# Optimization experiments

Hardware: AMD Instinct MI355X
Metric: run time of the kernel (lower is better)

The kernel has to match this reference:

```python
import jax, jax.numpy as jnp
import numpy as np

N_INPUTS = 128
N_LATENT = 21
LEN_TIME = 51
NUM_SHIFTS = 50
BATCH = 2048
N_HIDDEN = 4  # hidden relu layers in the outer DenseResBlock


def setup_inputs() -> dict:
    key = jax.random.key(0)
    ks = jax.random.split(key, 8)
    s = 0.05  # small init scale keeps activations sane through the residual stack
    return {
        "inputs": jax.random.normal(ks[0], (BATCH, LEN_TIME, N_INPUTS), jnp.float32),
        "L": jnp.eye(N_LATENT, dtype=jnp.float32)
             + s * jax.random.normal(ks[1], (N_LATENT, N_LATENT), jnp.float32),
        "ienc_W": s * jax.random.normal(ks[2], (N_INPUTS, N_LATENT), jnp.float32),
        "idec_W": s * jax.random.normal(ks[3], (N_LATENT, N_INPUTS), jnp.float32),
        "enc_W": s * jax.random.normal(ks[4], (N_HIDDEN, N_INPUTS, N_INPUTS), jnp.float32),
        "enc_b": jnp.zeros((N_HIDDEN, N_INPUTS), jnp.float32),
        "enc_Wo": s * jax.random.normal(ks[5], (N_INPUTS, N_INPUTS), jnp.float32),
        "enc_bo": jnp.zeros((N_INPUTS,), jnp.float32),
        "dec_W": s * jax.random.normal(ks[6], (N_HIDDEN, N_INPUTS, N_INPUTS), jnp.float32),
        "dec_b": jnp.zeros((N_HIDDEN, N_INPUTS), jnp.float32),
        "dec_Wo": s * jax.random.normal(ks[7], (N_INPUTS, N_INPUTS), jnp.float32),
        "dec_bo": jnp.zeros((N_INPUTS,), jnp.float32),
    }


def _resblock(x, W, b, Wo, bo):
    # DenseResBlock: stack of relu Dense layers + linear output + residual skip.
    h = x
    for i in range(W.shape[0]):  # fixed small layer count
        h = jax.nn.relu(h @ W[i] + b[i])
    return x + h @ Wo + bo


def reference(inputs, L, ienc_W, idec_W, enc_W, enc_b, enc_Wo, enc_bo,
              dec_W, dec_b, dec_Wo, dec_bo):
    B, T, n_in = inputs.shape
    len_pred = T - NUM_SHIFTS  # = 1

    auto_in = inputs.reshape(-1, n_in)                        # [B*T, n_in]
    pred_in = inputs[:, :len_pred, :].reshape(-1, n_in)       # [B*len_pred, n_in]

    # autoencoder path
    pe = _resblock(auto_in, enc_W, enc_b, enc_Wo, enc_bo)     # partially encoded
    fe = pe @ ienc_W                                          # fully encoded [., n_latent]
    pd = fe @ idec_W                                          # partially decoded
    autoencoder_output = _resblock(pd, dec_W, dec_b, dec_Wo, dec_bo)
    outer_auto_output = _resblock(pe, dec_W, dec_b, dec_Wo, dec_bo)

    # latent rollout: z_{k+1} = z_k @ L, decode every step
    pe_pred = _resblock(pred_in, enc_W, enc_b, enc_Wo, enc_bo)
    z0 = pe_pred @ ienc_W                                     # [B*len_pred, n_latent]

    def step(z, _):
        z_next = z @ L
        return z_next, z_next

    _, zs = jax.lax.scan(step, z0, None, length=NUM_SHIFTS)   # [S, B*len_pred, n_latent]

    # decode all shifts in one large batched pass (same math as per-shift decode)
    dec_in = zs.reshape(-1, zs.shape[-1]) @ idec_W            # [S*B*len_pred, n_in]
    dec_all = _resblock(dec_in, dec_W, dec_b, dec_Wo, dec_bo)
    predictions = (dec_all
                   .reshape(NUM_SHIFTS, B, len_pred, n_in)
                   .transpose(1, 0, 2, 3)
                   .reshape(B, NUM_SHIFTS * len_pred, n_in))

    return autoencoder_output, outer_auto_output, predictions
```

## Files before the change

kernel.cpp:

```cpp
#include <hip/hip_runtime.h>

#define NF 128
#define NLAT 21
#define NBATCH 2048
#define LEN_T 51
#define NSHIFT 50
#define AUTO_ROWS (NBATCH*LEN_T)
#define PRED_ROWS (NBATCH*NSHIFT)

typedef short bh8  __attribute__((ext_vector_type(8)));
typedef unsigned short us8 __attribute__((ext_vector_type(8)));
typedef float f32x4  __attribute__((ext_vector_type(4)));
typedef float f32x16 __attribute__((ext_vector_type(16)));

#define MFMA32(A,B,C) __builtin_amdgcn_mfma_f32_32x32x16_bf16(A,B,C,0,0,0)
#define SGB(m,n) __builtin_amdgcn_sched_group_barrier((m),(n),0)

__device__ __forceinline__ float bf2f(short s){
  unsigned u = ((unsigned)(unsigned short)s) << 16;
  return __builtin_bit_cast(float, u);
}
__device__ __forceinline__ short f2bf(float v){
  unsigned u = __builtin_bit_cast(unsigned, v);
  return (short)((u + 0x7FFFu + ((u>>16)&1u)) >> 16);
}

__global__ void k_mmul(const float* __restrict__ ienc, const float* __restrict__ idec,
                       float* __restrict__ M){
  int idx = blockIdx.x*256 + threadIdx.x;
  int i = idx>>7, j = idx&127;
  float s = 0.f;
#pragma unroll
  for(int k=0;k<NLAT;++k) s = fmaf(ienc[i*NLAT+k], idec[k*NF+j], s);
  M[idx] = s;
}

__global__ void k_prep(const float* __restrict__ encW, const float* __restrict__ encWo,
                       const float* __restrict__ decW, const float* __restrict__ decWo,
                       const float* __restrict__ M,    const float* __restrict__ idec,
                       unsigned short* __restrict__ swz){
  int id  = blockIdx.x*256 + threadIdx.x;
  int mat = id >> 11;
  int rem = id & 2047;
  int f   = rem >> 6, l = rem & 63;
  int s   = f >> 2,  mt = f & 3;
  int hl  = l >> 5,  c  = l & 31;
  const float* src;
  if(mat<4)       src = encW + mat*16384;
  else if(mat==4) src = encWo;
  else if(mat<9)  src = decW + (mat-5)*16384;
  else if(mat==9) src = decWo;
  else if(mat==10)src = M;
  else            src = idec;
  us8 w8;
#pragma unroll
  for(int i=0;i<8;++i){
    int k = s*16 + 4*hl + (i&3) + 8*(i>>2);
    float v;
    if(mat==11) v = (k<NLAT) ? src[k*NF + mt*32 + c] : 0.f;
    else        v = src[k*NF + mt*32 + c];
    w8[i] = (unsigned short)f2bf(v);
  }
  *(us8*)(swz + (size_t)mat*16384 + (size_t)f*512 + (size_t)l*8) = w8;
}

__device__ __forceinline__ void stage_issue(const unsigned short* g,
                                            unsigned short* lds, int wid, int lane){
  const unsigned short* gp = g + wid*512 + lane*8;
  unsigned short* lp = lds + wid*512;
#pragma unroll
  for(int i=0;i<8;++i){
    __builtin_amdgcn_global_load_lds(
      (const __attribute__((address_space(1))) void*)(gp + i*2048),
      (__attribute__((address_space(3))) void*)(lp + i*2048), 16, 0, 0);
  }
}

__device__ __forceinline__ void ldw4(const unsigned short* wl, int s, int lane, bh8 w[4]){
#pragma unroll
  for(int mt=0;mt<4;++mt) w[mt] = *(const bh8*)(wl + (s*4+mt)*512 + lane*8);
}
__device__ __forceinline__ void mm4(const bh8 w[4], bh8 b, f32x16 acc[4]){
#pragma unroll
  for(int mt=0;mt<4;++mt) acc[mt]=MFMA32(w[mt],b,acc[mt]);
}
__device__ __forceinline__ void run_layer(const unsigned short* wl,
    const bh8 h[8], f32x16 acc[4], int lane){
#pragma unroll
  for(int mt=0;mt<4;++mt){
    f32x16 z;
#pragma unroll
    for(int r=0;r<16;++r) z[r]=0.f;
    acc[mt]=z;
  }
  bh8 wA[4], wB[4];
  ldw4(wl,0,lane,wA);   SGB(0x100,4);
  ldw4(wl,1,lane,wB);   SGB(0x100,4);
  mm4(wA,h[0],acc);     SGB(0x8,4);
  ldw4(wl,2,lane,wA);   SGB(0x100,4);
  mm4(wB,h[1],acc);     SGB(0x8,4);
  ldw4(wl,3,lane,wB);   SGB(0x100,4);
  mm4(wA,h[2],acc);     SGB(0x8,4);
  ldw4(wl,4,lane,wA);   SGB(0x100,4);
  mm4(wB,h[3],acc);     SGB(0x8,4);
  ldw4(wl,5,lane,wB);   SGB(0x100,4);
  mm4(wA,h[4],acc);     SGB(0x8,4);
  ldw4(wl,6,lane,wA);   SGB(0x100,4);
  mm4(wB,h[5],acc);     SGB(0x8,4);
  ldw4(wl,7,lane,wB);   SGB(0x100,4);
  mm4(wA,h[6],acc);     SGB(0x8,4);
  mm4(wB,h[7],acc);     SGB(0x8,4);
}

__device__ __forceinline__ void epi_hidden(f32x16 acc[4], const float* bias,
    bh8 h[8], int hl){
#pragma unroll
  for(int mt=0;mt<4;++mt){
    f32x16 a = acc[mt];
#pragma unroll
    for(int q=0;q<4;++q){
      f32x4 b = *(const f32x4*)(bias + mt*32 + q*8 + hl*4);
#pragma unroll
      for(int j=0;j<4;++j) a[q*4+j]+=b[j];
    }
#pragma unroll
    for(int r=0;r<16;++r) a[r]=fmaxf(a[r],0.f);
#pragma unroll
    for(int p=0;p<2;++p){
      bh8 o;
#pragma unroll
      for(int i=0;i<8;++i) o[i]=f2bf(a[p*8 + (i>>2)*4 + (i&3)]);
      h[mt*2+p]=o;
    }
  }
}
__device__ __forceinline__ void epi_plain(f32x16 acc[4], bh8 h[8], int hl){
#pragma unroll
  for(int mt=0;mt<4;++mt){
    f32x16 a = acc[mt];
#pragma unroll
    for(int p=0;p<2;++p){
      bh8 o;
#pragma unroll
      for(int i=0;i<8;++i) o[i]=f2bf(a[p*8 + (i>>2)*4 + (i&3)]);
      h[mt*2+p]=o;
    }
  }
}

__device__ __forceinline__ void final_direct(float* __restrict__ rowptr,
    f32x16 acc[4], const float* bo, const bh8 res[8], int hl){
#pragma unroll
  for(int mt=0;mt<4;++mt){
    f32x16 a = acc[mt];
#pragma unroll
    for(int q=0;q<4;++q){
      f32x4 b = *(const f32x4*)(bo + mt*32 + q*8 + hl*4);
#pragma unroll
      for(int j=0;j<4;++j) a[q*4+j]+=b[j];
    }
    bh8 r0 = res[2*mt], r1 = res[2*mt+1];
#pragma unroll
    for(int r=0;r<16;++r){
      int i=((r>>2)&1)*4+(r&3);
      a[r] += bf2f(r<8 ? r0[i] : r1[i]);
    }
#pragma unroll
    for(int q=0;q<4;++q){
      f32x4 w; w[0]=a[q*4+0]; w[1]=a[q*4+1]; w[2]=a[q*4+2]; w[3]=a[q*4+3];
      *(f32x4*)(rowptr + mt*32 + q*8 + hl*4) = w;
    }
  }
}

__device__ __forceinline__ void dec_block(const unsigned short* __restrict__ swz,
    unsigned short (*wlds)[16384], int& cur, const float* bdec,
    bh8 h[8], f32x16 acc[4], const unsigned short* next_g,
    int wid, int lane, int hl){
#pragma unroll 1
  for(int l=0;l<4;++l){
    unsigned short* wc = cur ? wlds[1] : wlds[0];
    unsigned short* wn = cur ? wlds[0] : wlds[1];
    stage_issue(swz + (size_t)(l<3 ? 6+l : 9)*16384, wn, wid, lane);
    run_layer(wc, h, acc, lane);
    epi_hidden(acc, bdec + l*128, h, hl);
    __syncthreads(); cur^=1;
  }
  unsigned short* wc = cur ? wlds[1] : wlds[0];
  unsigned short* wn = cur ? wlds[0] : wlds[1];
  if(next_g) stage_issue(next_g, wn, wid, lane);
  run_layer(wc, h, acc, lane);
}

__global__ __launch_bounds__(256,2)
void k_main2(const float* __restrict__ gin, const unsigned short* __restrict__ swz,
             const float* __restrict__ encB, const float* __restrict__ encBo,
             const float* __restrict__ decB, const float* __restrict__ decBo,
             float* __restrict__ out1, float* __restrict__ out2, float* __restrict__ pe0){
  __shared__ __align__(16) unsigned short wlds[2][16384];
  __shared__ __align__(16) float blds[1280];
  const int tid=threadIdx.x, lane=tid&63, wid=tid>>6;
  const int hl=lane>>5, c31=lane&31;
  const int grow0=blockIdx.x*128;
  const int myrow=grow0 + wid*32 + c31;
  bh8 h[8], res[8];
  f32x16 acc[4];

  stage_issue(swz, wlds[0], wid, lane);
  for(int i=tid;i<512;i+=256) blds[i]      = encB[i];
  for(int i=tid;i<512;i+=256) blds[512+i]  = decB[i];
  if(tid<256) blds[1024+tid] = (tid<128) ? encBo[tid] : decBo[tid-128];

#pragma unroll
  for(int s=0;s<8;++s){
    f32x4 a=*(const f32x4*)(gin + (size_t)myrow*NF + s*16 + 4*hl);
    f32x4 b=*(const f32x4*)(gin + (size_t)myrow*NF + s*16 + 8 + 4*hl);
    bh8 o;
#pragma unroll
    for(int i=0;i<4;++i){ o[i]=f2bf(a[i]); o[i+4]=f2bf(b[i]); }
    h[s]=o; res[s]=o;
  }
  __syncthreads();
  int cur=0;

#pragma unroll 1
  for(int l=0;l<4;++l){
    unsigned short* wc = cur ? wlds[1] : wlds[0];
    unsigned short* wn = cur ? wlds[0] : wlds[1];
    stage_issue(swz + (size_t)(l+1)*16384, wn, wid, lane);
    run_layer(wc, h, acc, lane);
    epi_hidden(acc, blds + l*128, h, hl);
    __syncthreads(); cur^=1;
  }
  {
    unsigned short* wc = cur ? wlds[1] : wlds[0];
    unsigned short* wn = cur ? wlds[0] : wlds[1];
    stage_issue(swz + (size_t)5*16384, wn, wid, lane);
    run_layer(wc, h, acc, lane);
    int bidx = myrow / LEN_T;
    bool isz = (myrow == bidx*LEN_T);
#pragma unroll
    for(int mt=0;mt<4;++mt){
      f32x16 a = acc[mt];
#pragma unroll
      for(int q=0;q<4;++q){
        f32x4 b = *(const f32x4*)(blds + 1024 + mt*32 + q*8 + hl*4);
#pragma unroll
        for(int j=0;j<4;++j) a[q*4+j]+=b[j];
      }
      bh8 r0=res[2*mt], r1=res[2*mt+1];
#pragma unroll
      for(int r=0;r<16;++r){
        int i=((r>>2)&1)*4+(r&3);
        a[r] += bf2f(r<8 ? r0[i] : r1[i]);
      }
      if(isz){
#pragma unroll
        for(int q=0;q<4;++q){
          f32x4 w; w[0]=a[q*4+0]; w[1]=a[q*4+1]; w[2]=a[q*4+2]; w[3]=a[q*4+3];
          *(f32x4*)(pe0 + (size_t)bidx*NF + mt*32 + q*8 + hl*4) = w;
        }
      }
#pragma unroll
      for(int p=0;p<2;++p){
        bh8 o;
#pragma unroll
        for(int i=0;i<8;++i) o[i]=f2bf(a[p*8 + (i>>2)*4 + (i&3)]);
        h[mt*2+p]=o;
      }
    }
#pragma unroll
    for(int s=0;s<8;++s) res[s]=h[s];
    __syncthreads(); cur^=1;
  }

  dec_block(swz, wlds, cur, blds+512, h, acc, swz + (size_t)10*16384, wid, lane, hl);
  final_direct(out2 + (size_t)myrow*NF, acc, blds+1152, res, hl);
  __syncthreads(); cur^=1;

  {
    unsigned short* wc = cur ? wlds[1] : wlds[0];
    unsigned short* wn = cur ? wlds[0] : wlds[1];
    stage_issue(swz + (size_t)5*16384, wn, wid, lane);
    run_layer(wc, res, acc, lane);
    epi_plain(acc, h, hl);
#pragma unroll
    for(int s=0;s<8;++s) res[s]=h[s];
    __syncthreads(); cur^=1;
  }

  dec_block(swz, wlds, cur, blds+512, h, acc, nullptr, wid, lane, hl);
  final_direct(out1 + (size_t)myrow*NF, acc, blds+1152, res, hl);
}

__global__ void k_roll(const float* __restrict__ pe0, const float* __restrict__ ienc,
                       const float* __restrict__ L, float* __restrict__ zs){
  const int tid=threadIdx.x, lane=tid&63, wid=tid>>6, sub=lane&31, half=lane>>5;
  const int row=blockIdx.x*8 + wid*2 + half;
  const bool act = sub < NLAT;
  float Lc[NLAT];
#pragma unroll
  for(int k=0;k<NLAT;++k) Lc[k] = act ? L[k*NLAT+sub] : 0.f;
  float z=0.f;
  if(act){
    const float* pr = pe0 + (size_t)row*NF;
    float s0=0.f,s1=0.f,s2=0.f,s3=0.f;
#pragma unroll 8
    for(int k=0;k<NF;k+=4){
      s0=fmaf(pr[k+0], ienc[(k+0)*NLAT+sub], s0);
      s1=fmaf(pr[k+1], ienc[(k+1)*NLAT+sub], s1);
      s2=fmaf(pr[k+2], ienc[(k+2)*NLAT+sub], s2);
      s3=fmaf(pr[k+3], ienc[(k+3)*NLAT+sub], s3);
    }
    z=(s0+s1)+(s2+s3);
  }
  const int base = half*32;
#pragma unroll 1
  for(int s=0;s<NSHIFT;++s){
    float zn=0.f;
#pragma unroll
    for(int k=0;k<NLAT;++k) zn=fmaf(__shfl(z, base+k, 64), Lc[k], zn);
    z=zn;
    if(act) zs[((size_t)s*NBATCH + row)*NLAT + sub] = z;
  }
}

__global__ __launch_bounds__(256,2)
void k_pred2(const float* __restrict__ zs, const unsigned short* __restrict__ swz,
             const float* __restrict__ decB, const float* __restrict__ decBo,
             float* __restrict__ out3){
  __shared__ __align__(16) unsigned short wlds[2][16384];
  __shared__ __align__(16) float blds[1280];
  const int tid=threadIdx.x, lane=tid&63, wid=tid>>6;
  const int hl=lane>>5, c31=lane&31;
  const int grow0=blockIdx.x*128;
  const int prow=grow0 + wid*32 + c31;
  bh8 h[8], res[8];
  f32x16 acc[4];

  stage_issue(swz + (size_t)11*16384, wlds[0], wid, lane);
  for(int i=tid;i<512;i+=256) blds[512+i] = decB[i];
  if(tid<128) blds[1152+tid] = decBo[tid];

  bh8 zf[2];
  {
    const float* zr = zs + (size_t)prow*NLAT;
#pragma unroll
    for(int s=0;s<2;++s){
      bh8 o;
#pragma unroll
      for(int i=0;i<8;++i){
        int cc = s*16 + 4*hl + (i&3) + 8*(i>>2);
        o[i] = (cc<NLAT) ? f2bf(zr[cc]) : (short)0;
      }
      zf[s]=o;
    }
  }
  __syncthreads();
  int cur=0;

  {
    stage_issue(swz + (size_t)5*16384, wlds[1], wid, lane);
#pragma unroll
    for(int mt=0;mt<4;++mt){
      f32x16 z;
#pragma unroll
      for(int r=0;r<16;++r) z[r]=0.f;
      acc[mt]=z;
    }
    bh8 wA[4], wB[4];
    ldw4(wlds[0],0,lane,wA);  SGB(0x100,4);
    ldw4(wlds[0],1,lane,wB);  SGB(0x100,4);
    mm4(wA,zf[0],acc);        SGB(0x8,4);
    mm4(wB,zf[1],acc);        SGB(0x8,4);
    epi_plain(acc, h, hl);
#pragma unroll
    for(int s=0;s<8;++s) res[s]=h[s];
    __syncthreads(); cur^=1;
  }

  dec_block(swz, wlds, cur, blds+512, h, acc, nullptr, wid, lane, hl);

  int sh = prow >> 11, b = prow & 2047;
  final_direct(out3 + ((size_t)b*NSHIFT + sh)*NF, acc, blds+1152, res, hl);
}

extern "C" void kernel_launch(void* const* d_in, const int* in_sizes, int n_in,
                              void* d_out, int out_size, void* d_ws, size_t ws_size,
                              hipStream_t stream) {
  const float* gin   = (const float*)d_in[0];
  const float* L     = (const float*)d_in[1];
  const float* iencW = (const float*)d_in[2];
  const float* idecW = (const float*)d_in[3];
  const float* encW  = (const float*)d_in[4];
  const float* encB  = (const float*)d_in[5];
  const float* encWo = (const float*)d_in[6];
  const float* encBo = (const float*)d_in[7];
  const float* decW  = (const float*)d_in[8];
  const float* decB  = (const float*)d_in[9];
  const float* decWo = (const float*)d_in[10];
  const float* decBo = (const float*)d_in[11];

  float* out1 = (float*)d_out;
  float* out2 = out1 + (size_t)AUTO_ROWS*NF;
  float* out3 = out2 + (size_t)AUTO_ROWS*NF;

  float* M   = (float*)d_ws;
  float* pe0 = M + 16384;
  float* zs  = pe0 + (size_t)NBATCH*NF;
  unsigned short* swz = (unsigned short*)(zs + (size_t)NSHIFT*NBATCH*NLAT);

  hipLaunchKernelGGL(k_mmul, dim3(64),  dim3(256), 0, stream, iencW, idecW, M);
  hipLaunchKernelGGL(k_prep, dim3(96),  dim3(256), 0, stream, encW, encWo, decW, decWo, M, idecW, swz);
  hipLaunchKernelGGL(k_main2, dim3(AUTO_ROWS/128), dim3(256), 0, stream,
                     gin, swz, encB, encBo, decB, decBo, out1, out2, pe0);
  hipLaunchKernelGGL(k_roll, dim3(NBATCH/8), dim3(256), 0, stream, pe0, iencW, L, zs);
  hipLaunchKernelGGL(k_pred2, dim3(PRED_ROWS/128), dim3(256), 0, stream,
                     zs, swz, decB, decBo, out3);
}
```

Measured before the change: 165.6 us.

## Process 64 rows per wave, stash residuals in output buffers, pack bf16 conversions

```diff
diff --git a/kernel.cpp b/kernel.cpp
--- a/kernel.cpp
+++ b/kernel.cpp
@@ -9,9 +9,11 @@
 #define PRED_ROWS (NBATCH*NSHIFT)
 
 typedef short bh8  __attribute__((ext_vector_type(8)));
+typedef short bh4  __attribute__((ext_vector_type(4)));
 typedef unsigned short us8 __attribute__((ext_vector_type(8)));
 typedef float f32x4  __attribute__((ext_vector_type(4)));
 typedef float f32x16 __attribute__((ext_vector_type(16)));
+typedef unsigned u32x4 __attribute__((ext_vector_type(4)));
 
 #define MFMA32(A,B,C) __builtin_amdgcn_mfma_f32_32x32x16_bf16(A,B,C,0,0,0)
 #define SGB(m,n) __builtin_amdgcn_sched_group_barrier((m),(n),0)
@@ -23,6 +25,11 @@
 __device__ __forceinline__ short f2bf(float v){
   unsigned u = __builtin_bit_cast(unsigned, v);
   return (short)((u + 0x7FFFu + ((u>>16)&1u)) >> 16);
+}
+__device__ __forceinline__ unsigned pk2(float a, float b){
+  unsigned ua = __builtin_bit_cast(unsigned, a) + 0x8000u;
+  unsigned ub = __builtin_bit_cast(unsigned, b) + 0x8000u;
+  return (ua >> 16) | (ub & 0xFFFF0000u);
 }
 
 __global__ void k_mmul(const float* __restrict__ ienc, const float* __restrict__ idec,
@@ -76,221 +83,324 @@
   }
 }
 
-__device__ __forceinline__ void ldw4(const unsigned short* wl, int s, int lane, bh8 w[4]){
-#pragma unroll
-  for(int mt=0;mt<4;++mt) w[mt] = *(const bh8*)(wl + (s*4+mt)*512 + lane*8);
-}
-__device__ __forceinline__ void mm4(const bh8 w[4], bh8 b, f32x16 acc[4]){
-#pragma unroll
-  for(int mt=0;mt<4;++mt) acc[mt]=MFMA32(w[mt],b,acc[mt]);
-}
-__device__ __forceinline__ void run_layer(const unsigned short* wl,
-    const bh8 h[8], f32x16 acc[4], int lane){
-#pragma unroll
-  for(int mt=0;mt<4;++mt){
-    f32x16 z;
-#pragma unroll
-    for(int r=0;r<16;++r) z[r]=0.f;
-    acc[mt]=z;
-  }
-  bh8 wA[4], wB[4];
-  ldw4(wl,0,lane,wA);   SGB(0x100,4);
-  ldw4(wl,1,lane,wB);   SGB(0x100,4);
-  mm4(wA,h[0],acc);     SGB(0x8,4);
-  ldw4(wl,2,lane,wA);   SGB(0x100,4);
-  mm4(wB,h[1],acc);     SGB(0x8,4);
-  ldw4(wl,3,lane,wB);   SGB(0x100,4);
-  mm4(wA,h[2],acc);     SGB(0x8,4);
-  ldw4(wl,4,lane,wA);   SGB(0x100,4);
-  mm4(wB,h[3],acc);     SGB(0x8,4);
-  ldw4(wl,5,lane,wB);   SGB(0x100,4);
-  mm4(wA,h[4],acc);     SGB(0x8,4);
-  ldw4(wl,6,lane,wA);   SGB(0x100,4);
-  mm4(wB,h[5],acc);     SGB(0x8,4);
-  ldw4(wl,7,lane,wB);   SGB(0x100,4);
-  mm4(wA,h[6],acc);     SGB(0x8,4);
-  mm4(wB,h[7],acc);     SGB(0x8,4);
-}
-
-__device__ __forceinline__ void epi_hidden(f32x16 acc[4], const float* bias,
-    bh8 h[8], int hl){
-#pragma unroll
-  for(int mt=0;mt<4;++mt){
-    f32x16 a = acc[mt];
-#pragma unroll
-    for(int q=0;q<4;++q){
-      f32x4 b = *(const f32x4*)(bias + mt*32 + q*8 + hl*4);
-#pragma unroll
-      for(int j=0;j<4;++j) a[q*4+j]+=b[j];
-    }
-#pragma unroll
-    for(int r=0;r<16;++r) a[r]=fmaxf(a[r],0.f);
-#pragma unroll
-    for(int p=0;p<2;++p){
-      bh8 o;
-#pragma unroll
-      for(int i=0;i<8;++i) o[i]=f2bf(a[p*8 + (i>>2)*4 + (i&3)]);
-      h[mt*2+p]=o;
-    }
-  }
-}
-__device__ __forceinline__ void epi_plain(f32x16 acc[4], bh8 h[8], int hl){
-#pragma unroll
-  for(int mt=0;mt<4;++mt){
-    f32x16 a = acc[mt];
-#pragma unroll
-    for(int p=0;p<2;++p){
-      bh8 o;
-#pragma unroll
-      for(int i=0;i<8;++i) o[i]=f2bf(a[p*8 + (i>>2)*4 + (i&3)]);
-      h[mt*2+p]=o;
-    }
-  }
-}
-
-__device__ __forceinline__ void final_direct(float* __restrict__ rowptr,
-    f32x16 acc[4], const float* bo, const bh8 res[8], int hl){
-#pragma unroll
-  for(int mt=0;mt<4;++mt){
-    f32x16 a = acc[mt];
-#pragma unroll
-    for(int q=0;q<4;++q){
-      f32x4 b = *(const f32x4*)(bo + mt*32 + q*8 + hl*4);
-#pragma unroll
-      for(int j=0;j<4;++j) a[q*4+j]+=b[j];
-    }
-    bh8 r0 = res[2*mt], r1 = res[2*mt+1];
-#pragma unroll
-    for(int r=0;r<16;++r){
-      int i=((r>>2)&1)*4+(r&3);
-      a[r] += bf2f(r<8 ? r0[i] : r1[i]);
-    }
-#pragma unroll
-    for(int q=0;q<4;++q){
-      f32x4 w; w[0]=a[q*4+0]; w[1]=a[q*4+1]; w[2]=a[q*4+2]; w[3]=a[q*4+3];
-      *(f32x4*)(rowptr + mt*32 + q*8 + hl*4) = w;
-    }
-  }
-}
-
-__device__ __forceinline__ void dec_block(const unsigned short* __restrict__ swz,
-    unsigned short (*wlds)[16384], int& cur, const float* bdec,
-    bh8 h[8], f32x16 acc[4], const unsigned short* next_g,
-    int wid, int lane, int hl){
-#pragma unroll 1
-  for(int l=0;l<4;++l){
-    unsigned short* wc = cur ? wlds[1] : wlds[0];
-    unsigned short* wn = cur ? wlds[0] : wlds[1];
-    stage_issue(swz + (size_t)(l<3 ? 6+l : 9)*16384, wn, wid, lane);
-    run_layer(wc, h, acc, lane);
-    epi_hidden(acc, bdec + l*128, h, hl);
-    __syncthreads(); cur^=1;
-  }
-  unsigned short* wc = cur ? wlds[1] : wlds[0];
-  unsigned short* wn = cur ? wlds[0] : wlds[1];
-  if(next_g) stage_issue(next_g, wn, wid, lane);
-  run_layer(wc, h, acc, lane);
+__device__ __forceinline__ void run_half(const unsigned short* wl, int m,
+    const bh8 h[16], f32x16 acc[4], int lane){
+  f32x16 z;
+#pragma unroll
+  for(int r=0;r<16;++r) z[r]=0.f;
+  acc[0]=z; acc[1]=z; acc[2]=z; acc[3]=z;
+  const unsigned short* base = wl + m*1024 + lane*8;
+  bh8 a0 = *(const bh8*)(base);
+  bh8 a1 = *(const bh8*)(base + 512);
+#pragma unroll
+  for(int s=0;s<8;++s){
+    bh8 b0, b1;
+    if(s<7){
+      b0 = *(const bh8*)(base + (s+1)*2048);
+      b1 = *(const bh8*)(base + (s+1)*2048 + 512);
+      SGB(0x100,2);
+    }
+    __builtin_amdgcn_s_setprio(1);
+    acc[0]=MFMA32(a0,h[s],  acc[0]);
+    acc[1]=MFMA32(a1,h[s],  acc[1]);
+    acc[2]=MFMA32(a0,h[8+s],acc[2]);
+    acc[3]=MFMA32(a1,h[8+s],acc[3]);
+    __builtin_amdgcn_s_setprio(0);
+    SGB(0x8,4);
+    if(s<7){ a0=b0; a1=b1; }
+  }
+}
+
+__device__ __forceinline__ void run_half_k2(const unsigned short* wl, int m,
+    const bh8 zf[4], f32x16 acc[4], int lane){
+  f32x16 z;
+#pragma unroll
+  for(int r=0;r<16;++r) z[r]=0.f;
+  acc[0]=z; acc[1]=z; acc[2]=z; acc[3]=z;
+  const unsigned short* base = wl + m*1024 + lane*8;
+#pragma unroll
+  for(int s=0;s<2;++s){
+    bh8 a0 = *(const bh8*)(base + s*2048);
+    bh8 a1 = *(const bh8*)(base + s*2048 + 512);
+    acc[0]=MFMA32(a0,zf[s],  acc[0]);
+    acc[1]=MFMA32(a1,zf[s],  acc[1]);
+    acc[2]=MFMA32(a0,zf[2+s],acc[2]);
+    acc[3]=MFMA32(a1,zf[2+s],acc[3]);
+  }
+}
+
+__device__ __forceinline__ void epi_hidden_half(const f32x16 acc[4], const float* bl,
+    int m, int hl, bh8 out[8]){
+#pragma unroll
+  for(int t=0;t<2;++t){
+    f32x4 b[4];
+#pragma unroll
+    for(int q=0;q<4;++q) b[q] = *(const f32x4*)(bl + (2*m+t)*32 + q*8 + hl*4);
+#pragma unroll
+    for(int g=0;g<2;++g){
+      f32x16 a = acc[g*2+t];
+#pragma unroll
+      for(int q=0;q<4;++q)
+#pragma unroll
+        for(int j=0;j<4;++j) a[q*4+j] = fmaxf(a[q*4+j] + b[q][j], 0.f);
+#pragma unroll
+      for(int p=0;p<2;++p){
+        u32x4 w;
+#pragma unroll
+        for(int j=0;j<4;++j) w[j] = pk2(a[p*8+2*j], a[p*8+2*j+1]);
+        out[g*4+t*2+p] = __builtin_bit_cast(bh8, w);
+      }
+    }
+  }
+}
+__device__ __forceinline__ void epi_plain_half(const f32x16 acc[4], bh8 out[8]){
+#pragma unroll
+  for(int t=0;t<2;++t)
+#pragma unroll
+    for(int g=0;g<2;++g){
+      f32x16 a = acc[g*2+t];
+#pragma unroll
+      for(int p=0;p<2;++p){
+        u32x4 w;
+#pragma unroll
+        for(int j=0;j<4;++j) w[j] = pk2(a[p*8+2*j], a[p*8+2*j+1]);
+        out[g*4+t*2+p] = __builtin_bit_cast(bh8, w);
+      }
+    }
+}
+
+__device__ __forceinline__ void final_half(float* outp, size_t ro0, size_t ro1,
+    const f32x16 acc[4], const float* bo, const bh8 res[16], int m, int hl){
+#pragma unroll
+  for(int t=0;t<2;++t){
+    f32x4 b[4];
+#pragma unroll
+    for(int q=0;q<4;++q) b[q]=*(const f32x4*)(bo + (2*m+t)*32 + q*8 + hl*4);
+#pragma unroll
+    for(int g=0;g<2;++g){
+      f32x16 a = acc[g*2+t];
+      bh8 r0 = res[g*8+(2*m+t)*2], r1 = res[g*8+(2*m+t)*2+1];
+#pragma unroll
+      for(int q=0;q<4;++q)
+#pragma unroll
+        for(int j=0;j<4;++j){
+          int r=q*4+j;
+          a[r] += b[q][j] + bf2f((r<8 ? r0 : r1)[r&7]);
+        }
+      size_t ro = g ? ro1 : ro0;
+#pragma unroll
+      for(int q=0;q<4;++q){
+        f32x4 w; w[0]=a[q*4+0]; w[1]=a[q*4+1]; w[2]=a[q*4+2]; w[3]=a[q*4+3];
+        *(f32x4*)(outp + ro + (2*m+t)*32 + q*8 + hl*4) = w;
+      }
+    }
+  }
+}
+
+__device__ __forceinline__ void peWo_half(const f32x16 acc[4], const float* bo,
+    const bh8 res[16], int m, int hl, bh8 out[8], float* __restrict__ pe0,
+    int bidx0, int bidx1, bool isz0, bool isz1){
+#pragma unroll
+  for(int t=0;t<2;++t){
+    f32x4 b[4];
+#pragma unroll
+    for(int q=0;q<4;++q) b[q]=*(const f32x4*)(bo + (2*m+t)*32 + q*8 + hl*4);
+#pragma unroll
+    for(int g=0;g<2;++g){
+      f32x16 a = acc[g*2+t];
+      bh8 r0 = res[g*8+(2*m+t)*2], r1 = res[g*8+(2*m+t)*2+1];
+#pragma unroll
+      for(int q=0;q<4;++q)
+#pragma unroll
+        for(int j=0;j<4;++j){
+          int r=q*4+j;
+          a[r] += b[q][j] + bf2f((r<8 ? r0 : r1)[r&7]);
+        }
+      bool isz = g ? isz1 : isz0;
+      int bidx = g ? bidx1 : bidx0;
+      if(isz){
+#pragma unroll
+        for(int q=0;q<4;++q){
+          f32x4 w; w[0]=a[q*4+0]; w[1]=a[q*4+1]; w[2]=a[q*4+2]; w[3]=a[q*4+3];
+          *(f32x4*)(pe0 + (size_t)bidx*NF + (2*m+t)*32 + q*8 + hl*4) = w;
+        }
+      }
+#pragma unroll
+      for(int p=0;p<2;++p){
+        u32x4 w;
+#pragma unroll
+        for(int j=0;j<4;++j) w[j]=pk2(a[p*8+2*j], a[p*8+2*j+1]);
+        out[g*4+t*2+p]=__builtin_bit_cast(bh8,w);
+      }
+    }
+  }
+}
+
+__device__ __forceinline__ void layer_hidden(const unsigned short* wl, const float* bl,
+    bh8 h[16], int lane, int hl){
+  f32x16 acc[4]; bh8 t0[8], t1[8];
+  run_half(wl,0,h,acc,lane);
+  epi_hidden_half(acc,bl,0,hl,t0);
+  run_half(wl,1,h,acc,lane);
+  epi_hidden_half(acc,bl,1,hl,t1);
+#pragma unroll
+  for(int g=0;g<2;++g)
+#pragma unroll
+    for(int k=0;k<4;++k){ h[g*8+k]=t0[g*4+k]; h[g*8+4+k]=t1[g*4+k]; }
+}
+
+__device__ __forceinline__ void stash16(unsigned short* sp, const bh8 h[16], int lane){
+#pragma unroll
+  for(int f=0;f<16;++f) *(bh8*)(sp + f*512 + (size_t)lane*8) = h[f];
+}
+__device__ __forceinline__ void unstash16(const unsigned short* sp, bh8 r[16], int lane){
+#pragma unroll
+  for(int f=0;f<16;++f) r[f] = *(const bh8*)(sp + f*512 + (size_t)lane*8);
+}
+__device__ __forceinline__ void stash_rows(unsigned short* o3, const bh8 h[16],
+    int orow0, int orow1, int hl){
+#pragma unroll
+  for(int g=0;g<2;++g){
+    size_t rb = (size_t)(g?orow1:orow0)*256;
+#pragma unroll
+    for(int s=0;s<8;++s){
+      bh8 v=h[g*8+s];
+      bh4 lo=__builtin_shufflevector(v,v,0,1,2,3);
+      bh4 hi=__builtin_shufflevector(v,v,4,5,6,7);
+      *(bh4*)(o3 + rb + s*16 + 4*hl) = lo;
+      *(bh4*)(o3 + rb + s*16 + 8 + 4*hl) = hi;
+    }
+  }
+}
+__device__ __forceinline__ void unstash_rows(const unsigned short* o3, bh8 r[16],
+    int orow0, int orow1, int hl){
+#pragma unroll
+  for(int g=0;g<2;++g){
+    size_t rb=(size_t)(g?orow1:orow0)*256;
+#pragma unroll
+    for(int s=0;s<8;++s){
+      bh4 lo=*(const bh4*)(o3 + rb + s*16 + 4*hl);
+      bh4 hi=*(const bh4*)(o3 + rb + s*16 + 8 + 4*hl);
+      r[g*8+s]=__builtin_shufflevector(lo,hi,0,1,2,3,4,5,6,7);
+    }
+  }
 }
 
 __global__ __launch_bounds__(256,2)
-void k_main2(const float* __restrict__ gin, const unsigned short* __restrict__ swz,
+void k_main3(const float* __restrict__ gin, const unsigned short* __restrict__ swz,
              const float* __restrict__ encB, const float* __restrict__ encBo,
              const float* __restrict__ decB, const float* __restrict__ decBo,
-             float* __restrict__ out1, float* __restrict__ out2, float* __restrict__ pe0){
+             float* out1, float* out2, float* __restrict__ pe0){
   __shared__ __align__(16) unsigned short wlds[2][16384];
   __shared__ __align__(16) float blds[1280];
   const int tid=threadIdx.x, lane=tid&63, wid=tid>>6;
   const int hl=lane>>5, c31=lane&31;
-  const int grow0=blockIdx.x*128;
-  const int myrow=grow0 + wid*32 + c31;
-  bh8 h[8], res[8];
-  f32x16 acc[4];
+  const size_t rowbase = (size_t)blockIdx.x*256 + wid*64;
+  const int row0 = (int)rowbase + c31, row1 = row0 + 32;
+  unsigned short* st2 = (unsigned short*)out2 + rowbase*256;
+  unsigned short* st1 = (unsigned short*)out1 + rowbase*256;
+  const size_t ro0 = (size_t)row0*NF, ro1 = (size_t)row1*NF;
+  const int bidx0 = row0/LEN_T, bidx1 = row1/LEN_T;
+  const bool isz0 = (row0 == bidx0*LEN_T), isz1 = (row1 == bidx1*LEN_T);
+  bh8 h[16], res[16];
 
   stage_issue(swz, wlds[0], wid, lane);
-  for(int i=tid;i<512;i+=256) blds[i]      = encB[i];
-  for(int i=tid;i<512;i+=256) blds[512+i]  = decB[i];
-  if(tid<256) blds[1024+tid] = (tid<128) ? encBo[tid] : decBo[tid-128];
-
-#pragma unroll
-  for(int s=0;s<8;++s){
-    f32x4 a=*(const f32x4*)(gin + (size_t)myrow*NF + s*16 + 4*hl);
-    f32x4 b=*(const f32x4*)(gin + (size_t)myrow*NF + s*16 + 8 + 4*hl);
-    bh8 o;
-#pragma unroll
-    for(int i=0;i<4;++i){ o[i]=f2bf(a[i]); o[i+4]=f2bf(b[i]); }
-    h[s]=o; res[s]=o;
-  }
+  for(int i=tid;i<1280;i+=256)
+    blds[i] = (i<512)?encB[i] : (i<1024)?decB[i-512] : (i<1152)?encBo[i-1024] : decBo[i-1152];
+
+#pragma unroll
+  for(int g=0;g<2;++g){
+    const float* rp = gin + (g?ro1:ro0);
+#pragma unroll
+    for(int s=0;s<8;++s){
+      f32x4 a=*(const f32x4*)(rp + s*16 + 4*hl);
+      f32x4 b=*(const f32x4*)(rp + s*16 + 8 + 4*hl);
+      us8 o;
+#pragma unroll
+      for(int i=0;i<4;++i){ o[i]=(unsigned short)f2bf(a[i]); o[i+4]=(unsigned short)f2bf(b[i]); }
+      h[g*8+s]=__builtin_bit_cast(bh8,o);
+    }
+  }
+  stash16(st2, h, lane);
   __syncthreads();
   int cur=0;
 
 #pragma unroll 1
   for(int l=0;l<4;++l){
-    unsigned short* wc = cur ? wlds[1] : wlds[0];
-    unsigned short* wn = cur ? wlds[0] : wlds[1];
+    unsigned short* wc = cur?wlds[1]:wlds[0];
+    unsigned short* wn = cur?wlds[0]:wlds[1];
     stage_issue(swz + (size_t)(l+1)*16384, wn, wid, lane);
-    run_layer(wc, h, acc, lane);
-    epi_hidden(acc, blds + l*128, h, hl);
+    layer_hidden(wc, blds + l*NF, h, lane, hl);
     __syncthreads(); cur^=1;
   }
   {
-    unsigned short* wc = cur ? wlds[1] : wlds[0];
-    unsigned short* wn = cur ? wlds[0] : wlds[1];
+    unstash16(st2, res, lane);
+    unsigned short* wc = cur?wlds[1]:wlds[0];
+    unsigned short* wn = cur?wlds[0]:wlds[1];
     stage_issue(swz + (size_t)5*16384, wn, wid, lane);
-    run_layer(wc, h, acc, lane);
-    int bidx = myrow / LEN_T;
-    bool isz = (myrow == bidx*LEN_T);
-#pragma unroll
-    for(int mt=0;mt<4;++mt){
-      f32x16 a = acc[mt];
-#pragma unroll
-      for(int q=0;q<4;++q){
-        f32x4 b = *(const f32x4*)(blds + 1024 + mt*32 + q*8 + hl*4);
-#pragma unroll
-        for(int j=0;j<4;++j) a[q*4+j]+=b[j];
-      }
-      bh8 r0=res[2*mt], r1=res[2*mt+1];
-#pragma unroll
-      for(int r=0;r<16;++r){
-        int i=((r>>2)&1)*4+(r&3);
-        a[r] += bf2f(r<8 ? r0[i] : r1[i]);
-      }
-      if(isz){
-#pragma unroll
-        for(int q=0;q<4;++q){
-          f32x4 w; w[0]=a[q*4+0]; w[1]=a[q*4+1]; w[2]=a[q*4+2]; w[3]=a[q*4+3];
-          *(f32x4*)(pe0 + (size_t)bidx*NF + mt*32 + q*8 + hl*4) = w;
-        }
-      }
-#pragma unroll
-      for(int p=0;p<2;++p){
-        bh8 o;
-#pragma unroll
-        for(int i=0;i<8;++i) o[i]=f2bf(a[p*8 + (i>>2)*4 + (i&3)]);
-        h[mt*2+p]=o;
-      }
-    }
-#pragma unroll
-    for(int s=0;s<8;++s) res[s]=h[s];
-    __syncthreads(); cur^=1;
-  }
-
-  dec_block(swz, wlds, cur, blds+512, h, acc, swz + (size_t)10*16384, wid, lane, hl);
-  final_direct(out2 + (size_t)myrow*NF, acc, blds+1152, res, hl);
-  __syncthreads(); cur^=1;
-
+    f32x16 acc[4]; bh8 t0[8], t1[8];
+    run_half(wc,0,h,acc,lane);
+    peWo_half(acc, blds+1024, res, 0, hl, t0, pe0, bidx0,bidx1, isz0,isz1);
+    run_half(wc,1,h,acc,lane);
+    peWo_half(acc, blds+1024, res, 1, hl, t1, pe0, bidx0,bidx1, isz0,isz1);
+#pragma unroll
+    for(int g=0;g<2;++g)
+#pragma unroll
+      for(int k=0;k<4;++k){ h[g*8+k]=t0[g*4+k]; h[g*8+4+k]=t1[g*4+k]; }
+    stash16(st2, h, lane);
+    __syncthreads(); cur^=1;
+  }
+#pragma unroll 1
+  for(int l=0;l<4;++l){
+    unsigned short* wc = cur?wlds[1]:wlds[0];
+    unsigned short* wn = cur?wlds[0]:wlds[1];
+    stage_issue(swz + (size_t)(6+l)*16384, wn, wid, lane);
+    layer_hidden(wc, blds + 512 + l*NF, h, lane, hl);
+    __syncthreads(); cur^=1;
+  }
   {
-    unsigned short* wc = cur ? wlds[1] : wlds[0];
-    unsigned short* wn = cur ? wlds[0] : wlds[1];
+    unstash16(st2, res, lane);
+    unsigned short* wc = cur?wlds[1]:wlds[0];
+    unsigned short* wn = cur?wlds[0]:wlds[1];
+    stage_issue(swz + (size_t)10*16384, wn, wid, lane);
+    f32x16 acc[4];
+    run_half(wc,0,h,acc,lane);
+    final_half(out2, ro0, ro1, acc, blds+1152, res, 0, hl);
+    run_half(wc,1,h,acc,lane);
+    final_half(out2, ro0, ro1, acc, blds+1152, res, 1, hl);
+    __syncthreads(); cur^=1;
+  }
+  {
+    unsigned short* wc = cur?wlds[1]:wlds[0];
+    unsigned short* wn = cur?wlds[0]:wlds[1];
     stage_issue(swz + (size_t)5*16384, wn, wid, lane);
-    run_layer(wc, res, acc, lane);
-    epi_plain(acc, h, hl);
-#pragma unroll
-    for(int s=0;s<8;++s) res[s]=h[s];
-    __syncthreads(); cur^=1;
-  }
-
-  dec_block(swz, wlds, cur, blds+512, h, acc, nullptr, wid, lane, hl);
-  final_direct(out1 + (size_t)myrow*NF, acc, blds+1152, res, hl);
+    f32x16 acc[4]; bh8 t0[8], t1[8];
+    run_half(wc,0,res,acc,lane); epi_plain_half(acc,t0);
+    run_half(wc,1,res,acc,lane); epi_plain_half(acc,t1);
+#pragma unroll
+    for(int g=0;g<2;++g)
+#pragma unroll
+      for(int k=0;k<4;++k){ h[g*8+k]=t0[g*4+k]; h[g*8+4+k]=t1[g*4+k]; }
+    stash16(st1, h, lane);
+    __syncthreads(); cur^=1;
+  }
+#pragma unroll 1
+  for(int l=0;l<4;++l){
+    unsigned short* wc = cur?wlds[1]:wlds[0];
+    unsigned short* wn = cur?wlds[0]:wlds[1];
+    stage_issue(swz + (size_t)(6+l)*16384, wn, wid, lane);
+    layer_hidden(wc, blds + 512 + l*NF, h, lane, hl);
+    __syncthreads(); cur^=1;
+  }
+  {
+    unstash16(st1, res, lane);
+    unsigned short* wc = cur?wlds[1]:wlds[0];
+    f32x16 acc[4];
+    run_half(wc,0,h,acc,lane);
+    final_half(out1, ro0, ro1, acc, blds+1152, res, 0, hl);
+    run_half(wc,1,h,acc,lane);
+    final_half(out1, ro0, ro1, acc, blds+1152, res, 1, hl);
+  }
 }
 
 __global__ void k_roll(const float* __restrict__ pe0, const float* __restrict__ ienc,
@@ -326,63 +436,71 @@
 }
 
 __global__ __launch_bounds__(256,2)
-void k_pred2(const float* __restrict__ zs, const unsigned short* __restrict__ swz,
+void k_pred3(const float* __restrict__ zs, const unsigned short* __restrict__ swz,
              const float* __restrict__ decB, const float* __restrict__ decBo,
-             float* __restrict__ out3){
+             float* out3){
   __shared__ __align__(16) unsigned short wlds[2][16384];
-  __shared__ __align__(16) float blds[1280];
+  __shared__ __align__(16) float blds[640];
   const int tid=threadIdx.x, lane=tid&63, wid=tid>>6;
   const int hl=lane>>5, c31=lane&31;
-  const int grow0=blockIdx.x*128;
-  const int prow=grow0 + wid*32 + c31;
-  bh8 h[8], res[8];
-  f32x16 acc[4];
+  const size_t rowbase = (size_t)blockIdx.x*256 + wid*64;
+  const int prow0 = (int)rowbase + c31, prow1 = prow0 + 32;
+  const int orow0 = (prow0 & 2047)*NSHIFT + (prow0 >> 11);
+  const int orow1 = (prow1 & 2047)*NSHIFT + (prow1 >> 11);
+  bh8 h[16], res[16];
 
   stage_issue(swz + (size_t)11*16384, wlds[0], wid, lane);
-  for(int i=tid;i<512;i+=256) blds[512+i] = decB[i];
-  if(tid<128) blds[1152+tid] = decBo[tid];
-
-  bh8 zf[2];
-  {
-    const float* zr = zs + (size_t)prow*NLAT;
+  for(int i=tid;i<640;i+=256) blds[i] = (i<512) ? decB[i] : decBo[i-512];
+
+  bh8 zf[4];
+#pragma unroll
+  for(int g=0;g<2;++g){
+    const float* zr = zs + (size_t)(g?prow1:prow0)*NLAT;
 #pragma unroll
     for(int s=0;s<2;++s){
-      bh8 o;
+      us8 o;
 #pragma unroll
       for(int i=0;i<8;++i){
         int cc = s*16 + 4*hl + (i&3) + 8*(i>>2);
-        o[i] = (cc<NLAT) ? f2bf(zr[cc]) : (short)0;
+        o[i] = (cc<NLAT) ? (unsigned short)f2bf(zr[cc]) : (unsigned short)0;
       }
-      zf[s]=o;
+      zf[g*2+s]=__builtin_bit_cast(bh8,o);
     }
   }
   __syncthreads();
   int cur=0;
 
   {
-    stage_issue(swz + (size_t)5*16384, wlds[1], wid, lane);
-#pragma unroll
-    for(int mt=0;mt<4;++mt){
-      f32x16 z;
-#pragma unroll
-      for(int r=0;r<16;++r) z[r]=0.f;
-      acc[mt]=z;
-    }
-    bh8 wA[4], wB[4];
-    ldw4(wlds[0],0,lane,wA);  SGB(0x100,4);
-    ldw4(wlds[0],1,lane,wB);  SGB(0x100,4);
-    mm4(wA,zf[0],acc);        SGB(0x8,4);
-    mm4(wB,zf[1],acc);        SGB(0x8,4);
-    epi_plain(acc, h, hl);
-#pragma unroll
-    for(int s=0;s<8;++s) res[s]=h[s];
-    __syncthreads(); cur^=1;
-  }
-
-  dec_block(swz, wlds, cur, blds+512, h, acc, nullptr, wid, lane, hl);
-
-  int sh = prow >> 11, b = prow & 2047;
-  final_direct(out3 + ((size_t)b*NSHIFT + sh)*NF, acc, blds+1152, res, hl);
+    unsigned short* wc = wlds[0];
+    unsigned short* wn = wlds[1];
+    stage_issue(swz + (size_t)5*16384, wn, wid, lane);
+    f32x16 acc[4]; bh8 t0[8], t1[8];
+    run_half_k2(wc,0,zf,acc,lane); epi_plain_half(acc,t0);
+    run_half_k2(wc,1,zf,acc,lane); epi_plain_half(acc,t1);
+#pragma unroll
+    for(int g=0;g<2;++g)
+#pragma unroll
+      for(int k=0;k<4;++k){ h[g*8+k]=t0[g*4+k]; h[g*8+4+k]=t1[g*4+k]; }
+    stash_rows((unsigned short*)out3, h, orow0, orow1, hl);
+    __syncthreads(); cur=1;
+  }
+#pragma unroll 1
+  for(int l=0;l<4;++l){
+    unsigned short* wc = cur?wlds[1]:wlds[0];
+    unsigned short* wn = cur?wlds[0]:wlds[1];
+    stage_issue(swz + (size_t)(6+l)*16384, wn, wid, lane);
+    layer_hidden(wc, blds + l*NF, h, lane, hl);
+    __syncthreads(); cur^=1;
+  }
+  {
+    unstash_rows((const unsigned short*)out3, res, orow0, orow1, hl);
+    unsigned short* wc = cur?wlds[1]:wlds[0];
+    f32x16 acc[4];
+    run_half(wc,0,h,acc,lane);
+    final_half(out3, (size_t)orow0*NF, (size_t)orow1*NF, acc, blds+512, res, 0, hl);
+    run_half(wc,1,h,acc,lane);
+    final_half(out3, (size_t)orow0*NF, (size_t)orow1*NF, acc, blds+512, res, 1, hl);
+  }
 }
 
 extern "C" void kernel_launch(void* const* d_in, const int* in_sizes, int n_in,
@@ -412,9 +530,9 @@
 
   hipLaunchKernelGGL(k_mmul, dim3(64),  dim3(256), 0, stream, iencW, idecW, M);
   hipLaunchKernelGGL(k_prep, dim3(96),  dim3(256), 0, stream, encW, encWo, decW, decWo, M, idecW, swz);
-  hipLaunchKernelGGL(k_main2, dim3(AUTO_ROWS/128), dim3(256), 0, stream,
+  hipLaunchKernelGGL(k_main3, dim3(AUTO_ROWS/256), dim3(256), 0, stream,
                      gin, swz, encB, encBo, decB, decBo, out1, out2, pe0);
   hipLaunchKernelGGL(k_roll, dim3(NBATCH/8), dim3(256), 0, stream, pe0, iencW, L, zs);
-  hipLaunchKernelGGL(k_pred2, dim3(PRED_ROWS/128), dim3(256), 0, stream,
+  hipLaunchKernelGGL(k_pred3, dim3(PRED_ROWS/256), dim3(256), 0, stream,
                      zs, swz, decB, decBo, out3);
 }
```

New measurement: 170.4 us. +2.9%, slower.
